# Optimization experiments

Hardware: AMD Instinct MI355X
Metric: run time of the kernel (lower is better)

## Reference

```python
import jax, jax.numpy as jnp
import numpy as np

N_HEAD = 16
N_EMBD = 1024
B, T = 4, 2048


def setup_inputs() -> dict:
    key = jax.random.key(0)
    ks = jax.random.split(key, 5)
    s_in = 1.0 / np.sqrt(N_EMBD)
    return {
        "x": jax.random.normal(ks[0], (B, T, N_EMBD), dtype=jnp.float32),
        "W_qkv": jax.random.normal(ks[1], (N_EMBD, 3 * N_EMBD), dtype=jnp.float32) * s_in,
        "b_qkv": jnp.zeros((3 * N_EMBD,), dtype=jnp.float32),
        "W_proj": jax.random.normal(ks[2], (N_EMBD, N_EMBD), dtype=jnp.float32) * s_in,
        "b_proj": jnp.zeros((N_EMBD,), dtype=jnp.float32),
    }


def reference(x, W_qkv, b_qkv, W_proj, b_proj):
    Bb, Tt, C = x.shape
    H = N_HEAD
    hd = C // H  # head dim
    qkv = x @ W_qkv + b_qkv                      # [B,T,3C]
    q, k, v = jnp.split(qkv, 3, axis=-1)
    # [B,H,T,hd]
    q = q.reshape(Bb, Tt, H, hd).transpose(0, 2, 1, 3)
    k = k.reshape(Bb, Tt, H, hd).transpose(0, 2, 1, 3)
    v = v.reshape(Bb, Tt, H, hd).transpose(0, 2, 1, 3)
    scale = 1.0 / np.sqrt(hd).astype(np.float32)
    att = jnp.einsum("bhqd,bhkd->bhqk", q, k) * scale
    causal = jnp.tril(jnp.ones((Tt, Tt), dtype=bool))
    att = jnp.where(causal, att, jnp.float32(-jnp.inf))
    att = jax.nn.softmax(att, axis=-1)
    y = jnp.einsum("bhqk,bhkd->bhqd", att, v)    # [B,H,T,hd]
    y = y.transpose(0, 2, 1, 3).reshape(Bb, Tt, C)
    return y @ W_proj + b_proj
```

## Files before the change

### kernel.cpp

```cpp
#include <hip/hip_runtime.h>
#include <hip/hip_bf16.h>
#include <math.h>

typedef unsigned short u16;
typedef __bf16 bf16_t;
typedef bf16_t bf16x8 __attribute__((ext_vector_type(8)));
typedef float f32x4 __attribute__((ext_vector_type(4)));

#define N_HEADC 16
#define C_EMBD  1024
#define B_SZ    4
#define T_SEQ   2048
#define HD      64
#define M_TOT   (B_SZ * T_SEQ)

__device__ __forceinline__ u16 f2b(float f) {
    unsigned u = __float_as_uint(f);
    u = u + 0x7fffu + ((u >> 16) & 1u);
    return (u16)(u >> 16);
}
__device__ __forceinline__ unsigned pkbf16(float a, float b) {
    unsigned d;
    asm("v_cvt_pk_bf16_f32 %0, %1, %2" : "=v"(d) : "v"(a), "v"(b));
    return d;
}
__device__ __forceinline__ float fexp2(float x) {
#if __has_builtin(__builtin_amdgcn_exp2f)
    return __builtin_amdgcn_exp2f(x);
#else
    return exp2f(x);
#endif
}
__device__ __forceinline__ void gl_lds16(const u16* g, u16* l) {
    __builtin_amdgcn_global_load_lds(
        (const __attribute__((address_space(1))) unsigned int*)g,
        (__attribute__((address_space(3))) unsigned int*)l,
        16, 0, 0);
}


__global__ __launch_bounds__(256) void cast_f32_to_bf16(const float* __restrict__ in,
                                                        u16* __restrict__ out) {
    int i = (blockIdx.x * 256 + threadIdx.x) * 4;
    float4 v = *(const float4*)(in + i);
    ushort4 o;
    o.x = f2b(v.x); o.y = f2b(v.y); o.z = f2b(v.z); o.w = f2b(v.w);
    *(ushort4*)(out + i) = o;
}

__global__ __launch_bounds__(256) void transpose_cast(const float* __restrict__ in,
                                                      u16* __restrict__ out,
                                                      int K, int N) {
    __shared__ float tile[32][33];
    int n0 = blockIdx.x * 32, k0 = blockIdx.y * 32;
    for (int i = threadIdx.y; i < 32; i += 8)
        tile[i][threadIdx.x] = in[(size_t)(k0 + i) * N + n0 + threadIdx.x];
    __syncthreads();
    for (int i = threadIdx.y; i < 32; i += 8)
        out[(size_t)(n0 + i) * K + k0 + threadIdx.x] = f2b(tile[threadIdx.x][i]);
}

__global__ __launch_bounds__(256) void transpose_v(const u16* __restrict__ qV,
                                                   u16* __restrict__ qVt) {
    __shared__ u16 tile[64][66];
    int t0 = blockIdx.x * 64;
    size_t base = (size_t)blockIdx.y * T_SEQ * HD;
    int tid = threadIdx.x;
    #pragma unroll
    for (int c = 0; c < 2; ++c) {
        int ch = tid * 2 + c;
        int row = ch >> 3, off = (ch & 7) * 8;
        uint4 v = *(const uint4*)&qV[base + (size_t)(t0 + row) * HD + off];
        const unsigned* pv = (const unsigned*)&v;
        #pragma unroll
        for (int e = 0; e < 4; ++e)
            *(unsigned*)&tile[row][off + e * 2] = pv[e];
    }
    __syncthreads();
    int d = tid >> 2, tq = tid & 3;
    u16 vals[16];
    #pragma unroll
    for (int k = 0; k < 16; ++k) vals[k] = tile[tq * 16 + k][d];
    *(uint4*)&qVt[base + (size_t)d * T_SEQ + t0 + tq * 16] = *(uint4*)&vals[0];
    *(uint4*)&qVt[base + (size_t)d * T_SEQ + t0 + tq * 16 + 8] = *(uint4*)&vals[8];
}

__device__ __forceinline__ void stage_tile(const u16* __restrict__ A,
                                           const u16* __restrict__ BT,
                                           int rowA0, int rowB0, int k0,
                                           u16* sA, u16* sB, int w, int lane) {
    int srow = lane >> 2, sko = (lane & 3) * 8;
    #pragma unroll
    for (int c = 0; c < 2; ++c) {
        int rb = (w * 2 + c) * 16;
        gl_lds16(&A[(size_t)(rowA0 + rb + srow) * C_EMBD + k0 + sko], &sA[rb * 32]);
    }
    #pragma unroll
    for (int c = 0; c < 2; ++c) {
        int rb = (w * 2 + c) * 16;
        gl_lds16(&BT[(size_t)(rowB0 + rb + srow) * C_EMBD + k0 + sko], &sB[rb * 32]);
    }
}

__global__ __launch_bounds__(256) void gemm_qkv(const u16* __restrict__ A,
                                                const u16* __restrict__ BT,
                                                const float* __restrict__ bias,
                                                u16* __restrict__ qQ,
                                                u16* __restrict__ qK,
                                                u16* __restrict__ qV) {
    const int NK = C_EMBD / 32;
    __shared__ __align__(16) u16 sA[2][128 * 32];
    __shared__ __align__(16) u16 sB[2][128 * 32];
    int m0 = blockIdx.y * 128;
    int n0 = blockIdx.x * 128;
    int tid = threadIdx.x;
    int w = tid >> 6, lane = tid & 63;
    int m_off = (w & 1) * 64, n_off = (w >> 1) * 64;
    int quad = lane >> 4, rl = lane & 15;

    f32x4 acc[4][4];
    #pragma unroll
    for (int i = 0; i < 4; ++i)
        #pragma unroll
        for (int j = 0; j < 4; ++j)
            acc[i][j] = f32x4{0.f, 0.f, 0.f, 0.f};

    stage_tile(A, BT, m0, n0, 0, sA[0], sB[0], w, lane);

    for (int kt = 0; kt < NK; ++kt) {
        __syncthreads();
        if (kt + 1 < NK)
            stage_tile(A, BT, m0, n0, (kt + 1) * 32,
                       sA[(kt + 1) & 1], sB[(kt + 1) & 1], w, lane);
        const u16* pA = sA[kt & 1];
        const u16* pB = sB[kt & 1];
        bf16x8 af[4], bfr[4];
        #pragma unroll
        for (int i = 0; i < 4; ++i)
            af[i] = *(const bf16x8*)&pA[(m_off + i * 16 + rl) * 32 + quad * 8];
        #pragma unroll
        for (int j = 0; j < 4; ++j)
            bfr[j] = *(const bf16x8*)&pB[(n_off + j * 16 + rl) * 32 + quad * 8];
        #pragma unroll
        for (int i = 0; i < 4; ++i)
            #pragma unroll
            for (int j = 0; j < 4; ++j)
                acc[i][j] = __builtin_amdgcn_mfma_f32_16x16x32_bf16(af[i], bfr[j], acc[i][j], 0, 0, 0);
    }

    const float QSC = 0.18033688011112042f;
    #pragma unroll
    for (int j = 0; j < 4; ++j) {
        int n = n0 + n_off + j * 16 + rl;
        float bv = bias[n];
        int p = n >> 10, cch = n & 1023;
        int h = cch >> 6, d = cch & 63;
        u16* dst = p == 0 ? qQ : (p == 1 ? qK : qV);
        float sc = p == 0 ? QSC : 1.0f;
        #pragma unroll
        for (int i = 0; i < 4; ++i) {
            int mbase = m0 + m_off + i * 16 + quad * 4;
            int bb = mbase >> 11, t0 = mbase & 2047;
            size_t thbase = ((size_t)bb * N_HEADC + h) * T_SEQ;
            #pragma unroll
            for (int r = 0; r < 4; ++r)
                dst[(thbase + t0 + r) * HD + d] = f2b((acc[i][j][r] + bv) * sc);
        }
    }
}

__global__ __launch_bounds__(256) void gemm_proj(const u16* __restrict__ A,
                                                 const u16* __restrict__ BT,
                                                 const float* __restrict__ bias,
                                                 float* __restrict__ out) {
    const int NK = C_EMBD / 32;
    __shared__ __align__(16) u16 sA[2][128 * 32];
    __shared__ __align__(16) u16 sB[2][128 * 32];
    int m0 = blockIdx.y * 128;
    int n0 = blockIdx.x * 128;
    int tid = threadIdx.x;
    int w = tid >> 6, lane = tid & 63;
    int m_off = (w & 1) * 64, n_off = (w >> 1) * 64;
    int quad = lane >> 4, rl = lane & 15;

    f32x4 acc[4][4];
    #pragma unroll
    for (int i = 0; i < 4; ++i)
        #pragma unroll
        for (int j = 0; j < 4; ++j)
            acc[i][j] = f32x4{0.f, 0.f, 0.f, 0.f};

    stage_tile(A, BT, m0, n0, 0, sA[0], sB[0], w, lane);

    for (int kt = 0; kt < NK; ++kt) {
        __syncthreads();
        if (kt + 1 < NK)
            stage_tile(A, BT, m0, n0, (kt + 1) * 32,
                       sA[(kt + 1) & 1], sB[(kt + 1) & 1], w, lane);
        const u16* pA = sA[kt & 1];
        const u16* pB = sB[kt & 1];
        bf16x8 af[4], bfr[4];
        #pragma unroll
        for (int i = 0; i < 4; ++i)
            af[i] = *(const bf16x8*)&pA[(m_off + i * 16 + rl) * 32 + quad * 8];
        #pragma unroll
        for (int j = 0; j < 4; ++j)
            bfr[j] = *(const bf16x8*)&pB[(n_off + j * 16 + rl) * 32 + quad * 8];
        #pragma unroll
        for (int i = 0; i < 4; ++i)
            #pragma unroll
            for (int j = 0; j < 4; ++j)
                acc[i][j] = __builtin_amdgcn_mfma_f32_16x16x32_bf16(af[i], bfr[j], acc[i][j], 0, 0, 0);
    }

    #pragma unroll
    for (int i = 0; i < 4; ++i) {
        int mbase = m0 + m_off + i * 16 + quad * 4;
        #pragma unroll
        for (int j = 0; j < 4; ++j) {
            int n = n0 + n_off + j * 16 + rl;
            float bv = bias[n];
            #pragma unroll
            for (int r = 0; r < 4; ++r)
                out[(size_t)(mbase + r) * C_EMBD + n] = acc[i][j][r] + bv;
        }
    }
}

__global__ __launch_bounds__(256) void attn_mfma(const u16* __restrict__ Qg,
                                                 const u16* __restrict__ Kg,
                                                 const u16* __restrict__ Vtg,
                                                 u16* __restrict__ yb) {
    int bx = blockIdx.x, h = blockIdx.y, b = blockIdx.z;
    const size_t hs = (size_t)T_SEQ * HD;
    const u16* Qp  = Qg  + ((size_t)b * N_HEADC + h) * hs;
    const u16* Kp  = Kg  + ((size_t)b * N_HEADC + h) * hs;
    const u16* Vtp = Vtg + ((size_t)b * N_HEADC + h) * hs;

    __shared__ __align__(16) u16 sK[2][2][64][32];
    __shared__ __align__(16) u16 sVt[2][2][64][32];
    __shared__ __align__(16) u16 sP[4][32][72];

    int tid = threadIdx.x;
    int lane = tid & 63, w = tid >> 6;
    int quad = lane >> 4, rl = lane & 15;
    u16* sPw = &sP[w][0][0];
    int srow = lane >> 2;
    int sch = (lane & 3) * 8;
    const f32x4 mneg = {-16.f, -16.f, -16.f, -16.f};

    #pragma unroll
    for (int phase = 0; phase < 2; ++phase) {
        int qt = phase == 0 ? (15 - bx) : bx;
        int q0w = qt * 128 + w * 32;
        int nkt = 2 * qt + 2;

        bf16x8 qf[2][2];
        #pragma unroll
        for (int nt = 0; nt < 2; ++nt)
            #pragma unroll
            for (int ks = 0; ks < 2; ++ks)
                qf[nt][ks] = *(const bf16x8*)&Qp[(size_t)(q0w + nt * 16 + rl) * HD + ks * 32 + quad * 8];

        f32x4 O[2][4];
        #pragma unroll
        for (int mi = 0; mi < 2; ++mi)
            #pragma unroll
            for (int nd = 0; nd < 4; ++nd)
                O[mi][nd] = f32x4{0.f, 0.f, 0.f, 0.f};
        float l_[2] = {0.f, 0.f};

        __syncthreads();
        #pragma unroll
        for (int c = 0; c < 4; ++c) {
            int lc = w * 4 + c;
            int ks = (lc >> 2) & 1;
            int rb = (lc & 3) * 16;
            if (lc < 8)
                gl_lds16(Kp + (size_t)(rb + srow) * HD + ks * 32 + sch, &sK[0][ks][rb][0]);
            else
                gl_lds16(Vtp + (size_t)(rb + srow) * T_SEQ + ks * 32 + sch, &sVt[0][ks][rb][0]);
        }

        for (int kt = 0; kt < nkt; ++kt) {
            __syncthreads();
            int buf = kt & 1;
            int k0 = kt * 64;
            if (kt + 1 < nkt) {
                int k1 = k0 + 64;
                #pragma unroll
                for (int c = 0; c < 4; ++c) {
                    int lc = w * 4 + c;
                    int ks = (lc >> 2) & 1;
                    int rb = (lc & 3) * 16;
                    if (lc < 8)
                        gl_lds16(Kp + (size_t)(k1 + rb + srow) * HD + ks * 32 + sch,
                                 &sK[buf ^ 1][ks][rb][0]);
                    else
                        gl_lds16(Vtp + (size_t)(rb + srow) * T_SEQ + k1 + ks * 32 + sch,
                                 &sVt[buf ^ 1][ks][rb][0]);
                }
            }
            if (k0 > q0w + 31) continue;

            f32x4 st[4][2];
            #pragma unroll
            for (int mt = 0; mt < 4; ++mt) {
                bf16x8 ak0 = *(const bf16x8*)&sK[buf][0][mt * 16 + rl][quad * 8];
                bf16x8 ak1 = *(const bf16x8*)&sK[buf][1][mt * 16 + rl][quad * 8];
                #pragma unroll
                for (int nt = 0; nt < 2; ++nt) {
                    f32x4 t = __builtin_amdgcn_mfma_f32_16x16x32_bf16(ak0, qf[nt][0], mneg, 0, 0, 0);
                    st[mt][nt] = __builtin_amdgcn_mfma_f32_16x16x32_bf16(ak1, qf[nt][1], t, 0, 0, 0);
                }
            }

            if (k0 + 63 > q0w) {
                #pragma unroll
                for (int mt = 0; mt < 4; ++mt)
                    #pragma unroll
                    for (int nt = 0; nt < 2; ++nt)
                        #pragma unroll
                        for (int r = 0; r < 4; ++r) {
                            int kpos = k0 + mt * 16 + quad * 4 + r;
                            int q = q0w + nt * 16 + rl;
                            if (kpos > q) st[mt][nt][r] = -INFINITY;
                        }
            }

            #pragma unroll
            for (int nt = 0; nt < 2; ++nt) {
                float lsum = 0.f;
                #pragma unroll
                for (int mt = 0; mt < 4; ++mt) {
                    float p0 = fexp2(st[mt][nt][0]);
                    float p1 = fexp2(st[mt][nt][1]);
                    float p2 = fexp2(st[mt][nt][2]);
                    float p3 = fexp2(st[mt][nt][3]);
                    lsum += (p0 + p1) + (p2 + p3);
                    *(uint2*)&sPw[(nt * 16 + rl) * 72 + mt * 16 + quad * 4] =
                        make_uint2(pkbf16(p0, p1), pkbf16(p2, p3));
                }
                l_[nt] += lsum;
            }

            #pragma unroll
            for (int ks = 0; ks < 2; ++ks) {
                bf16x8 ap0 = *(const bf16x8*)&sPw[(0 * 16 + rl) * 72 + ks * 32 + quad * 8];
                bf16x8 ap1 = *(const bf16x8*)&sPw[(1 * 16 + rl) * 72 + ks * 32 + quad * 8];
                #pragma unroll
                for (int nd = 0; nd < 4; ++nd) {
                    bf16x8 bv = *(const bf16x8*)&sVt[buf][ks][nd * 16 + rl][quad * 8];
                    O[0][nd] = __builtin_amdgcn_mfma_f32_16x16x32_bf16(ap0, bv, O[0][nd], 0, 0, 0);
                    O[1][nd] = __builtin_amdgcn_mfma_f32_16x16x32_bf16(ap1, bv, O[1][nd], 0, 0, 0);
                }
            }
        }

        #pragma unroll
        for (int nt = 0; nt < 2; ++nt) {
            l_[nt] += __shfl_xor(l_[nt], 16);
            l_[nt] += __shfl_xor(l_[nt], 32);
        }
        float linv[2] = {1.f / l_[0], 1.f / l_[1]};
        int idxq = quad * 4;
        #pragma unroll
        for (int mi = 0; mi < 2; ++mi)
            #pragma unroll
            for (int r = 0; r < 4; ++r) {
                float li = __shfl(linv[mi], idxq + r);
                int qg = q0w + mi * 16 + quad * 4 + r;
                size_t base = ((size_t)b * T_SEQ + qg) * C_EMBD + h * HD;
                #pragma unroll
                for (int nd = 0; nd < 4; ++nd)
                    yb[base + nd * 16 + rl] = f2b(O[mi][nd][r] * li);
            }
    }
}

extern "C" void kernel_launch(void* const* d_in, const int* in_sizes, int n_in,
                              void* d_out, int out_size, void* d_ws, size_t ws_size,
                              hipStream_t stream) {
    const float* x     = (const float*)d_in[0];
    const float* Wqkv  = (const float*)d_in[1];
    const float* bqkv  = (const float*)d_in[2];
    const float* Wproj = (const float*)d_in[3];
    const float* bproj = (const float*)d_in[4];
    float* out = (float*)d_out;

    char* ws = (char*)d_ws;
    u16* xb     = (u16*)(ws);
    u16* WqkvT  = (u16*)(ws + (size_t)16 * 1024 * 1024);
    u16* WprojT = (u16*)(ws + (size_t)22 * 1024 * 1024);
    u16* qQ     = (u16*)(ws + (size_t)24 * 1024 * 1024);
    u16* qK     = (u16*)(ws + (size_t)40 * 1024 * 1024);
    u16* qVt    = (u16*)(ws + (size_t)56 * 1024 * 1024);
    u16* yb     = (u16*)(ws + (size_t)72 * 1024 * 1024);
    u16* qV     = yb;

    cast_f32_to_bf16<<<dim3(M_TOT * C_EMBD / (256 * 4)), dim3(256), 0, stream>>>(x, xb);
    transpose_cast<<<dim3(3 * C_EMBD / 32, C_EMBD / 32), dim3(32, 8), 0, stream>>>(
        Wqkv, WqkvT, C_EMBD, 3 * C_EMBD);
    transpose_cast<<<dim3(C_EMBD / 32, C_EMBD / 32), dim3(32, 8), 0, stream>>>(
        Wproj, WprojT, C_EMBD, C_EMBD);
    gemm_qkv<<<dim3(3 * C_EMBD / 128, M_TOT / 128), dim3(256), 0, stream>>>(
        xb, WqkvT, bqkv, qQ, qK, qV);
    transpose_v<<<dim3(T_SEQ / 64, B_SZ * N_HEADC), dim3(256), 0, stream>>>(qV, qVt);
    attn_mfma<<<dim3(8, N_HEADC, B_SZ), dim3(256), 0, stream>>>(
        qQ, qK, qVt, yb);
    gemm_proj<<<dim3(C_EMBD / 128, M_TOT / 128), dim3(256), 0, stream>>>(
        yb, WprojT, bproj, out);
}
```

Before: 274.7 us.

## Fuse prep kernels, write V transposed from QKV GEMM, precompute load pointers

Three input cast/transpose kernels are merged into a single prep launch. The QKV GEMM epilogue now writes V directly in transposed layout through an LDS tile, which removes the separate transpose_v kernel and its round trip through global memory. The GEMM and attention loops also precompute per-wave global and LDS pointers and advance them by a fixed stride, replacing per-iteration index arithmetic. Together these cut launch count and global traffic, at the cost of extra barriers in the V epilogue.

```diff
diff --git a/kernel.cpp b/kernel.cpp
--- a/kernel.cpp
+++ b/kernel.cpp
@@ -38,68 +38,37 @@
         16, 0, 0);
 }
 
-
-__global__ __launch_bounds__(256) void cast_f32_to_bf16(const float* __restrict__ in,
-                                                        u16* __restrict__ out) {
-    int i = (blockIdx.x * 256 + threadIdx.x) * 4;
-    float4 v = *(const float4*)(in + i);
-    ushort4 o;
-    o.x = f2b(v.x); o.y = f2b(v.y); o.z = f2b(v.z); o.w = f2b(v.w);
-    *(ushort4*)(out + i) = o;
-}
-
-__global__ __launch_bounds__(256) void transpose_cast(const float* __restrict__ in,
-                                                      u16* __restrict__ out,
-                                                      int K, int N) {
+__global__ __launch_bounds__(256) void prep(const float* __restrict__ x,
+                                            const float* __restrict__ Wqkv,
+                                            const float* __restrict__ Wproj,
+                                            u16* __restrict__ xb,
+                                            u16* __restrict__ WqkvT,
+                                            u16* __restrict__ WprojT) {
     __shared__ float tile[32][33];
-    int n0 = blockIdx.x * 32, k0 = blockIdx.y * 32;
-    for (int i = threadIdx.y; i < 32; i += 8)
-        tile[i][threadIdx.x] = in[(size_t)(k0 + i) * N + n0 + threadIdx.x];
+    int bid = blockIdx.x, tid = threadIdx.x;
+    if (bid < 8192) {
+        int i = bid * 1024 + tid * 4;
+        float4 v = *(const float4*)(x + i);
+        ushort4 o;
+        o.x = f2b(v.x); o.y = f2b(v.y); o.z = f2b(v.z); o.w = f2b(v.w);
+        *(ushort4*)(xb + i) = o;
+        return;
+    }
+    const float* in; u16* outp; int N, bx, by;
+    if (bid < 8192 + 3072) {
+        int b2 = bid - 8192; bx = b2 % 96; by = b2 / 96;
+        in = Wqkv; outp = WqkvT; N = 3 * C_EMBD;
+    } else {
+        int b2 = bid - 11264; bx = b2 % 32; by = b2 / 32;
+        in = Wproj; outp = WprojT; N = C_EMBD;
+    }
+    int tx = tid & 31, ty = tid >> 5;
+    int n0 = bx * 32, k0 = by * 32;
+    for (int i = ty; i < 32; i += 8)
+        tile[i][tx] = in[(size_t)(k0 + i) * N + n0 + tx];
     __syncthreads();
-    for (int i = threadIdx.y; i < 32; i += 8)
-        out[(size_t)(n0 + i) * K + k0 + threadIdx.x] = f2b(tile[threadIdx.x][i]);
-}
-
-__global__ __launch_bounds__(256) void transpose_v(const u16* __restrict__ qV,
-                                                   u16* __restrict__ qVt) {
-    __shared__ u16 tile[64][66];
-    int t0 = blockIdx.x * 64;
-    size_t base = (size_t)blockIdx.y * T_SEQ * HD;
-    int tid = threadIdx.x;
-    #pragma unroll
-    for (int c = 0; c < 2; ++c) {
-        int ch = tid * 2 + c;
-        int row = ch >> 3, off = (ch & 7) * 8;
-        uint4 v = *(const uint4*)&qV[base + (size_t)(t0 + row) * HD + off];
-        const unsigned* pv = (const unsigned*)&v;
-        #pragma unroll
-        for (int e = 0; e < 4; ++e)
-            *(unsigned*)&tile[row][off + e * 2] = pv[e];
-    }
-    __syncthreads();
-    int d = tid >> 2, tq = tid & 3;
-    u16 vals[16];
-    #pragma unroll
-    for (int k = 0; k < 16; ++k) vals[k] = tile[tq * 16 + k][d];
-    *(uint4*)&qVt[base + (size_t)d * T_SEQ + t0 + tq * 16] = *(uint4*)&vals[0];
-    *(uint4*)&qVt[base + (size_t)d * T_SEQ + t0 + tq * 16 + 8] = *(uint4*)&vals[8];
-}
-
-__device__ __forceinline__ void stage_tile(const u16* __restrict__ A,
-                                           const u16* __restrict__ BT,
-                                           int rowA0, int rowB0, int k0,
-                                           u16* sA, u16* sB, int w, int lane) {
-    int srow = lane >> 2, sko = (lane & 3) * 8;
-    #pragma unroll
-    for (int c = 0; c < 2; ++c) {
-        int rb = (w * 2 + c) * 16;
-        gl_lds16(&A[(size_t)(rowA0 + rb + srow) * C_EMBD + k0 + sko], &sA[rb * 32]);
-    }
-    #pragma unroll
-    for (int c = 0; c < 2; ++c) {
-        int rb = (w * 2 + c) * 16;
-        gl_lds16(&BT[(size_t)(rowB0 + rb + srow) * C_EMBD + k0 + sko], &sB[rb * 32]);
-    }
+    for (int i = ty; i < 32; i += 8)
+        outp[(size_t)(n0 + i) * C_EMBD + k0 + tx] = f2b(tile[tx][i]);
 }
 
 __global__ __launch_bounds__(256) void gemm_qkv(const u16* __restrict__ A,
@@ -107,16 +76,16 @@
                                                 const float* __restrict__ bias,
                                                 u16* __restrict__ qQ,
                                                 u16* __restrict__ qK,
-                                                u16* __restrict__ qV) {
+                                                u16* __restrict__ qVt) {
     const int NK = C_EMBD / 32;
-    __shared__ __align__(16) u16 sA[2][128 * 32];
-    __shared__ __align__(16) u16 sB[2][128 * 32];
+    __shared__ __align__(16) u16 sS[2][2][128 * 32];
     int m0 = blockIdx.y * 128;
     int n0 = blockIdx.x * 128;
     int tid = threadIdx.x;
     int w = tid >> 6, lane = tid & 63;
     int m_off = (w & 1) * 64, n_off = (w >> 1) * 64;
     int quad = lane >> 4, rl = lane & 15;
+    int srow = lane >> 2, sko = (lane & 3) * 8;
 
     f32x4 acc[4][4];
     #pragma unroll
@@ -125,15 +94,26 @@
         for (int j = 0; j < 4; ++j)
             acc[i][j] = f32x4{0.f, 0.f, 0.f, 0.f};
 
-    stage_tile(A, BT, m0, n0, 0, sA[0], sB[0], w, lane);
+    const u16* gA0 = A + (size_t)(m0 + w * 32 + srow) * C_EMBD + sko;
+    const u16* gA1 = gA0 + 16 * C_EMBD;
+    const u16* gB0 = BT + (size_t)(n0 + w * 32 + srow) * C_EMBD + sko;
+    const u16* gB1 = gB0 + 16 * C_EMBD;
+    u16* lA[2] = { &sS[0][0][w * 32 * 32], &sS[1][0][w * 32 * 32] };
+    u16* lB[2] = { &sS[0][1][w * 32 * 32], &sS[1][1][w * 32 * 32] };
+
+    gl_lds16(gA0, lA[0]); gl_lds16(gA1, lA[0] + 512);
+    gl_lds16(gB0, lB[0]); gl_lds16(gB1, lB[0] + 512);
 
     for (int kt = 0; kt < NK; ++kt) {
         __syncthreads();
-        if (kt + 1 < NK)
-            stage_tile(A, BT, m0, n0, (kt + 1) * 32,
-                       sA[(kt + 1) & 1], sB[(kt + 1) & 1], w, lane);
-        const u16* pA = sA[kt & 1];
-        const u16* pB = sB[kt & 1];
+        if (kt + 1 < NK) {
+            gA0 += 32; gA1 += 32; gB0 += 32; gB1 += 32;
+            int nb = (kt + 1) & 1;
+            gl_lds16(gA0, lA[nb]); gl_lds16(gA1, lA[nb] + 512);
+            gl_lds16(gB0, lB[nb]); gl_lds16(gB1, lB[nb] + 512);
+        }
+        const u16* pA = &sS[kt & 1][0][0];
+        const u16* pB = &sS[kt & 1][1][0];
         bf16x8 af[4], bfr[4];
         #pragma unroll
         for (int i = 0; i < 4; ++i)
@@ -149,22 +129,55 @@
     }
 
     const float QSC = 0.18033688011112042f;
-    #pragma unroll
-    for (int j = 0; j < 4; ++j) {
-        int n = n0 + n_off + j * 16 + rl;
-        float bv = bias[n];
-        int p = n >> 10, cch = n & 1023;
-        int h = cch >> 6, d = cch & 63;
-        u16* dst = p == 0 ? qQ : (p == 1 ? qK : qV);
+    int p = n0 >> 10;
+    if (p < 2) {
+        u16* dst = p == 0 ? qQ : qK;
         float sc = p == 0 ? QSC : 1.0f;
         #pragma unroll
-        for (int i = 0; i < 4; ++i) {
-            int mbase = m0 + m_off + i * 16 + quad * 4;
-            int bb = mbase >> 11, t0 = mbase & 2047;
-            size_t thbase = ((size_t)bb * N_HEADC + h) * T_SEQ;
-            #pragma unroll
-            for (int r = 0; r < 4; ++r)
-                dst[(thbase + t0 + r) * HD + d] = f2b((acc[i][j][r] + bv) * sc);
+        for (int j = 0; j < 4; ++j) {
+            int n = n0 + n_off + j * 16 + rl;
+            float bv = bias[n];
+            int cch = n & 1023;
+            int h = cch >> 6, d = cch & 63;
+            #pragma unroll
+            for (int i = 0; i < 4; ++i) {
+                int mbase = m0 + m_off + i * 16 + quad * 4;
+                int bb = mbase >> 11, t0 = mbase & 2047;
+                size_t thbase = ((size_t)bb * N_HEADC + h) * T_SEQ;
+                #pragma unroll
+                for (int r = 0; r < 4; ++r)
+                    dst[(thbase + t0 + r) * HD + d] = f2b((acc[i][j][r] + bv) * sc);
+            }
+        }
+    } else {
+        u16 (*tr)[136] = (u16 (*)[136])&sS[0][0][0];
+        int bb = m0 >> 11, t0g = m0 & 2047;
+        #pragma unroll
+        for (int half = 0; half < 2; ++half) {
+            __syncthreads();
+            if (n_off == half * 64) {
+                #pragma unroll
+                for (int j = 0; j < 4; ++j) {
+                    int rowr = j * 16 + rl;
+                    float bv = bias[n0 + half * 64 + rowr];
+                    #pragma unroll
+                    for (int i = 0; i < 4; ++i) {
+                        int mm = m_off + i * 16 + quad * 4;
+                        *(unsigned*)&tr[rowr][mm]     = pkbf16(acc[i][j][0] + bv, acc[i][j][1] + bv);
+                        *(unsigned*)&tr[rowr][mm + 2] = pkbf16(acc[i][j][2] + bv, acc[i][j][3] + bv);
+                    }
+                }
+            }
+            __syncthreads();
+            #pragma unroll
+            for (int s = 0; s < 4; ++s) {
+                int task = s * 256 + tid;
+                int nn = task >> 4, seg = task & 15;
+                int n = (n0 & 1023) + half * 64 + nn;
+                int h = n >> 6, d = n & 63;
+                size_t di = (((size_t)bb * N_HEADC + h) * HD + d) * T_SEQ + t0g + seg * 8;
+                *(uint4*)&qVt[di] = *(const uint4*)&tr[nn][seg * 8];
+            }
         }
     }
 }
@@ -174,14 +187,14 @@
                                                  const float* __restrict__ bias,
                                                  float* __restrict__ out) {
     const int NK = C_EMBD / 32;
-    __shared__ __align__(16) u16 sA[2][128 * 32];
-    __shared__ __align__(16) u16 sB[2][128 * 32];
+    __shared__ __align__(16) u16 sS[2][2][128 * 32];
     int m0 = blockIdx.y * 128;
     int n0 = blockIdx.x * 128;
     int tid = threadIdx.x;
     int w = tid >> 6, lane = tid & 63;
     int m_off = (w & 1) * 64, n_off = (w >> 1) * 64;
     int quad = lane >> 4, rl = lane & 15;
+    int srow = lane >> 2, sko = (lane & 3) * 8;
 
     f32x4 acc[4][4];
     #pragma unroll
@@ -190,15 +203,26 @@
         for (int j = 0; j < 4; ++j)
             acc[i][j] = f32x4{0.f, 0.f, 0.f, 0.f};
 
-    stage_tile(A, BT, m0, n0, 0, sA[0], sB[0], w, lane);
+    const u16* gA0 = A + (size_t)(m0 + w * 32 + srow) * C_EMBD + sko;
+    const u16* gA1 = gA0 + 16 * C_EMBD;
+    const u16* gB0 = BT + (size_t)(n0 + w * 32 + srow) * C_EMBD + sko;
+    const u16* gB1 = gB0 + 16 * C_EMBD;
+    u16* lA[2] = { &sS[0][0][w * 32 * 32], &sS[1][0][w * 32 * 32] };
+    u16* lB[2] = { &sS[0][1][w * 32 * 32], &sS[1][1][w * 32 * 32] };
+
+    gl_lds16(gA0, lA[0]); gl_lds16(gA1, lA[0] + 512);
+    gl_lds16(gB0, lB[0]); gl_lds16(gB1, lB[0] + 512);
 
     for (int kt = 0; kt < NK; ++kt) {
         __syncthreads();
-        if (kt + 1 < NK)
-            stage_tile(A, BT, m0, n0, (kt + 1) * 32,
-                       sA[(kt + 1) & 1], sB[(kt + 1) & 1], w, lane);
-        const u16* pA = sA[kt & 1];
-        const u16* pB = sB[kt & 1];
+        if (kt + 1 < NK) {
+            gA0 += 32; gA1 += 32; gB0 += 32; gB1 += 32;
+            int nb = (kt + 1) & 1;
+            gl_lds16(gA0, lA[nb]); gl_lds16(gA1, lA[nb] + 512);
+            gl_lds16(gB0, lB[nb]); gl_lds16(gB1, lB[nb] + 512);
+        }
+        const u16* pA = &sS[kt & 1][0][0];
+        const u16* pB = &sS[kt & 1][1][0];
         bf16x8 af[4], bfr[4];
         #pragma unroll
         for (int i = 0; i < 4; ++i)
@@ -249,6 +273,27 @@
     int sch = (lane & 3) * 8;
     const f32x4 mneg = {-16.f, -16.f, -16.f, -16.f};
 
+    const u16* gp0[4];
+    u16* ld0[4]; u16* ld1[4];
+    int gstep;
+    if (w < 2) {
+        gstep = 64 * HD;
+        #pragma unroll
+        for (int c = 0; c < 4; ++c) {
+            gp0[c] = Kp + (size_t)(c * 16 + srow) * HD + w * 32 + sch;
+            ld0[c] = &sK[0][w][c * 16][0];
+            ld1[c] = &sK[1][w][c * 16][0];
+        }
+    } else {
+        gstep = 64;
+        #pragma unroll
+        for (int c = 0; c < 4; ++c) {
+            gp0[c] = Vtp + (size_t)(c * 16 + srow) * T_SEQ + (w - 2) * 32 + sch;
+            ld0[c] = &sVt[0][w - 2][c * 16][0];
+            ld1[c] = &sVt[1][w - 2][c * 16][0];
+        }
+    }
+
     #pragma unroll
     for (int phase = 0; phase < 2; ++phase) {
         int qt = phase == 0 ? (15 - bx) : bx;
@@ -270,35 +315,24 @@
                 O[mi][nd] = f32x4{0.f, 0.f, 0.f, 0.f};
         float l_[2] = {0.f, 0.f};
 
+        const u16* gp[4];
+        #pragma unroll
+        for (int c = 0; c < 4; ++c) gp[c] = gp0[c];
+
         __syncthreads();
         #pragma unroll
-        for (int c = 0; c < 4; ++c) {
-            int lc = w * 4 + c;
-            int ks = (lc >> 2) & 1;
-            int rb = (lc & 3) * 16;
-            if (lc < 8)
-                gl_lds16(Kp + (size_t)(rb + srow) * HD + ks * 32 + sch, &sK[0][ks][rb][0]);
-            else
-                gl_lds16(Vtp + (size_t)(rb + srow) * T_SEQ + ks * 32 + sch, &sVt[0][ks][rb][0]);
-        }
+        for (int c = 0; c < 4; ++c) gl_lds16(gp[c], ld0[c]);
 
         for (int kt = 0; kt < nkt; ++kt) {
             __syncthreads();
             int buf = kt & 1;
             int k0 = kt * 64;
             if (kt + 1 < nkt) {
-                int k1 = k0 + 64;
+                u16* const* ldn = ((kt + 1) & 1) ? ld1 : ld0;
                 #pragma unroll
                 for (int c = 0; c < 4; ++c) {
-                    int lc = w * 4 + c;
-                    int ks = (lc >> 2) & 1;
-                    int rb = (lc & 3) * 16;
-                    if (lc < 8)
-                        gl_lds16(Kp + (size_t)(k1 + rb + srow) * HD + ks * 32 + sch,
-                                 &sK[buf ^ 1][ks][rb][0]);
-                    else
-                        gl_lds16(Vtp + (size_t)(rb + srow) * T_SEQ + k1 + ks * 32 + sch,
-                                 &sVt[buf ^ 1][ks][rb][0]);
+                    gp[c] += gstep;
+                    gl_lds16(gp[c], ldn[c]);
                 }
             }
             if (k0 > q0w + 31) continue;
@@ -396,16 +430,10 @@
     u16* qK     = (u16*)(ws + (size_t)40 * 1024 * 1024);
     u16* qVt    = (u16*)(ws + (size_t)56 * 1024 * 1024);
     u16* yb     = (u16*)(ws + (size_t)72 * 1024 * 1024);
-    u16* qV     = yb;
-
-    cast_f32_to_bf16<<<dim3(M_TOT * C_EMBD / (256 * 4)), dim3(256), 0, stream>>>(x, xb);
-    transpose_cast<<<dim3(3 * C_EMBD / 32, C_EMBD / 32), dim3(32, 8), 0, stream>>>(
-        Wqkv, WqkvT, C_EMBD, 3 * C_EMBD);
-    transpose_cast<<<dim3(C_EMBD / 32, C_EMBD / 32), dim3(32, 8), 0, stream>>>(
-        Wproj, WprojT, C_EMBD, C_EMBD);
+
+    prep<<<dim3(12288), dim3(256), 0, stream>>>(x, Wqkv, Wproj, xb, WqkvT, WprojT);
     gemm_qkv<<<dim3(3 * C_EMBD / 128, M_TOT / 128), dim3(256), 0, stream>>>(
-        xb, WqkvT, bqkv, qQ, qK, qV);
-    transpose_v<<<dim3(T_SEQ / 64, B_SZ * N_HEADC), dim3(256), 0, stream>>>(qV, qVt);
+        xb, WqkvT, bqkv, qQ, qK, qVt);
     attn_mfma<<<dim3(8, N_HEADC, B_SZ), dim3(256), 0, stream>>>(
         qQ, qK, qVt, yb);
     gemm_proj<<<dim3(C_EMBD / 128, M_TOT / 128), dim3(256), 0, stream>>>(
```

After: 259.1 us. 5.7% less time.
